# Performance work log

Hardware: AMD Instinct MI355X
Metric: run time of the kernel (lower is better)

## Reference

```python
import jax, jax.numpy as jnp
import numpy as np

D_MODEL = 1024
D_Q = 1024
D_K = 1024
D_V = 1024
B, S = 4, 2048


def setup_inputs() -> dict:
    key = jax.random.key(0)
    kx, kq, kk, kv = jax.random.split(key, 4)
    # torch Linear(in, out) weight is [out, in]; y = x @ W.T. Use kaiming-ish scale.
    sc = 1.0 / np.sqrt(D_MODEL)
    x = jax.random.normal(kx, (B, S, D_MODEL), dtype=jnp.float32)
    Wq = jax.random.normal(kq, (D_Q, D_MODEL), dtype=jnp.float32) * sc
    Wk = jax.random.normal(kk, (D_K, D_MODEL), dtype=jnp.float32) * sc
    Wv = jax.random.normal(kv, (D_V, D_MODEL), dtype=jnp.float32) * sc
    return {"x": x, "Wq": Wq, "Wk": Wk, "Wv": Wv}


def reference(x, Wq, Wk, Wv):
    d_k = Wk.shape[0]
    q = jnp.einsum('bsd,qd->bsq', x, Wq)  # [B,S,d_q]
    k = jnp.einsum('bsd,kd->bsk', x, Wk)  # [B,S,d_k]
    v = jnp.einsum('bsd,vd->bsv', x, Wv)  # [B,S,d_v]
    scores = jnp.einsum('bqd,bkd->bqk', q, k) / jnp.sqrt(jnp.float32(d_k))
    seq = scores.shape[-1]
    causal = jnp.tril(jnp.ones((seq, seq), dtype=bool))  # True = keep
    scores = jnp.where(causal[None, :, :], scores, -jnp.inf)
    probs = jax.nn.softmax(scores, axis=-1)
    return jnp.einsum('bqk,bkv->bqv', probs, v)
```

## Files before the change

kernel.cpp:

```cpp
#include <hip/hip_runtime.h>
#include <hip/hip_bf16.h>
#include <stdint.h>

typedef __attribute__((ext_vector_type(8))) short short8;
typedef __attribute__((ext_vector_type(4))) float floatx4;

typedef const __attribute__((address_space(1))) void* gvp;
typedef __attribute__((address_space(3))) void* lvp;

__device__ __forceinline__ unsigned short f2bf(float f) {
    unsigned u = __float_as_uint(f);
    u += 0x7fffu + ((u >> 16) & 1u);
    return (unsigned short)(u >> 16);
}

#define BAR()    do { asm volatile("" ::: "memory"); __builtin_amdgcn_s_barrier(); asm volatile("" ::: "memory"); } while (0)
#define WAITL()  do { asm volatile("s_waitcnt lgkmcnt(0)" ::: "memory"); __builtin_amdgcn_sched_barrier(0); } while (0)
#define WAITV4() asm volatile("s_waitcnt vmcnt(4)" ::: "memory")
#define WAITV0() asm volatile("s_waitcnt vmcnt(0)" ::: "memory")

__global__ __launch_bounds__(256)
void cvt_all(const float* __restrict__ x, const float* __restrict__ wq,
             const float* __restrict__ wk, const float* __restrict__ wv,
             unsigned short* __restrict__ Xb, unsigned short* __restrict__ WqT,
             unsigned short* __restrict__ WkT, unsigned short* __restrict__ Wvb) {
    const int b = blockIdx.x, t = threadIdx.x;
    if (b < 2304) {
        const float* in; unsigned short* out; long base;
        if (b < 2048) { in = x;  out = Xb;  base = (long)b * 1024; }
        else          { in = wv; out = Wvb; base = (long)(b - 2048) * 1024; }
        #pragma unroll
        for (int k = 0; k < 4; ++k) {
            long idx = base + k * 256 + t;
            float4 v = reinterpret_cast<const float4*>(in)[idx];
            uint2 o;
            o.x = (unsigned)f2bf(v.x) | ((unsigned)f2bf(v.y) << 16);
            o.y = (unsigned)f2bf(v.z) | ((unsigned)f2bf(v.w) << 16);
            reinterpret_cast<uint2*>(out)[idx] = o;
        }
    } else {
        const int bb = b - 2304;
        const float* in = (bb < 256) ? wq : wk;
        unsigned short* out = (bb < 256) ? WqT : WkT;
        const int tile = bb & 255;
        const int e0 = (tile >> 4) * 64, d0 = (tile & 15) * 64;
        __shared__ unsigned short ldsT[64][68];
        const int r = t >> 4, cq = t & 15;
        #pragma unroll
        for (int p = 0; p < 4; ++p) {
            const int e = p * 16 + r;
            float4 v = *reinterpret_cast<const float4*>(in + (long)(e0 + e) * 1024 + d0 + cq * 4);
            ldsT[cq*4+0][e] = f2bf(v.x);
            ldsT[cq*4+1][e] = f2bf(v.y);
            ldsT[cq*4+2][e] = f2bf(v.z);
            ldsT[cq*4+3][e] = f2bf(v.w);
        }
        __syncthreads();
        #pragma unroll
        for (int p = 0; p < 4; ++p) {
            const int d = p * 16 + r;
            ushort4 o = *reinterpret_cast<const ushort4*>(&ldsT[d][cq * 4]);
            *reinterpret_cast<ushort4*>(out + (long)(d0 + d) * 1024 + e0 + cq * 4) = o;
        }
    }
}

__device__ __forceinline__ void stage_tile(unsigned short* Abuf, unsigned short* Bbuf,
                                           const unsigned short* A, int lda,
                                           const unsigned short* B, int ldb, int k0,
                                           int wid, int srow, int piece) {
    #pragma unroll
    for (int i = 0; i < 4; ++i) {
        const int c = wid * 4 + i;
        const int row = c * 8 + srow;
        const int cs = (piece * 16) ^ ((row & 7) << 4);
        __builtin_amdgcn_global_load_lds(
            (gvp)(reinterpret_cast<const char*>(A + (long)row * lda + k0) + cs),
            (lvp)(reinterpret_cast<char*>(Abuf) + c * 1024), 16, 0, 0);
        __builtin_amdgcn_global_load_lds(
            (gvp)(reinterpret_cast<const char*>(B + (long)row * ldb + k0) + cs),
            (lvp)(reinterpret_cast<char*>(Bbuf) + c * 1024), 16, 0, 0);
    }
}

__device__ __forceinline__ void compute_tile(floatx4 acc[4][4], const unsigned short* As,
                                             const unsigned short* Bs, int wm, int wn,
                                             int frow, int lane) {
    #pragma unroll
    for (int ks = 0; ks < 2; ++ks) {
        short8 af[4], bf[4];
        const int colb = ks * 64 + (lane >> 4) * 16;
        #pragma unroll
        for (int i = 0; i < 4; ++i) {
            const int ar = wm + i * 16 + frow;
            af[i] = *reinterpret_cast<const short8*>(
                reinterpret_cast<const char*>(As) + ar * 128 + (colb ^ ((ar & 7) << 4)));
            const int br = wn + i * 16 + frow;
            bf[i] = *reinterpret_cast<const short8*>(
                reinterpret_cast<const char*>(Bs) + br * 128 + (colb ^ ((br & 7) << 4)));
        }
        #pragma unroll
        for (int i = 0; i < 4; ++i)
            #pragma unroll
            for (int j = 0; j < 4; ++j)
                acc[i][j] = __builtin_amdgcn_mfma_f32_16x16x32_bf16(af[i], bf[j], acc[i][j], 0, 0, 0);
    }
}

__global__ __launch_bounds__(256, 2)
void g_chunk(const unsigned short* __restrict__ WkT, const unsigned short* __restrict__ WqT,
             float* __restrict__ Gw) {
    const int bx = blockIdx.x, by = blockIdx.y, bz = blockIdx.z;
    const unsigned short* A = WkT + (long)by * 128 * 1024;
    const unsigned short* B = WqT + (long)bx * 128 * 1024;

    __shared__ unsigned short As[2][128 * 64];
    __shared__ unsigned short Bs[2][128 * 64];

    const int tid = threadIdx.x, lane = tid & 63, wid = tid >> 6;
    const int srow = lane >> 3, piece = lane & 7;
    const int wm = (wid >> 1) * 64, wn = (wid & 1) * 64, frow = lane & 15;

    floatx4 acc[4][4] = {};
    const int kbase = bz * 256;

    stage_tile(As[0], Bs[0], A, 1024, B, 1024, kbase, wid, srow, piece);
    WAITV0(); BAR();
    int cur = 0;
    #pragma unroll 1
    for (int t = 0; t < 4; ++t) {
        if (t < 3)
            stage_tile(As[cur ^ 1], Bs[cur ^ 1], A, 1024, B, 1024, kbase + (t + 1) * 64,
                       wid, srow, piece);
        compute_tile(acc, As[cur], Bs[cur], wm, wn, frow, lane);
        WAITV0(); BAR();
        cur ^= 1;
    }

    float* Cb = Gw + (long)bz * (1 << 20) + (long)(by * 128) * 1024 + bx * 128;
    const int cr0 = wm + (lane >> 4) * 4;
    const int cc0 = wn + (lane & 15);
    #pragma unroll
    for (int i = 0; i < 4; ++i)
        #pragma unroll
        for (int j = 0; j < 4; ++j)
            #pragma unroll
            for (int r = 0; r < 4; ++r)
                Cb[(long)(cr0 + i * 16 + r) * 1024 + cc0 + j * 16] = acc[i][j][r];
}

__global__ __launch_bounds__(256)
void reduce_g(const float* __restrict__ Gw, unsigned short* __restrict__ Gp) {
    const long i4 = (long)blockIdx.x * 256 + threadIdx.x;
    const long M4 = (1l << 20) / 4;
    float4 a = reinterpret_cast<const float4*>(Gw)[i4];
    float4 b = reinterpret_cast<const float4*>(Gw)[i4 + M4];
    float4 c = reinterpret_cast<const float4*>(Gw)[i4 + 2 * M4];
    float4 d = reinterpret_cast<const float4*>(Gw)[i4 + 3 * M4];
    float sx = (a.x + b.x + c.x + d.x) * 0.03125f;
    float sy = (a.y + b.y + c.y + d.y) * 0.03125f;
    float sz = (a.z + b.z + c.z + d.z) * 0.03125f;
    float sw = (a.w + b.w + c.w + d.w) * 0.03125f;
    uint2 o;
    o.x = (unsigned)f2bf(sx) | ((unsigned)f2bf(sy) << 16);
    o.y = (unsigned)f2bf(sz) | ((unsigned)f2bf(sw) << 16);
    reinterpret_cast<uint2*>(Gp)[i4] = o;
}

__global__ __launch_bounds__(256, 2)
void pv_sched(const unsigned short* __restrict__ P, const unsigned short* __restrict__ Vt,
              float* __restrict__ out) {
    const int flat = (blockIdx.z * 8 + blockIdx.y) * 8 + blockIdx.x;
    const int xcd = flat & 7, lid = flat >> 3;
    const int bz = xcd >> 1, parity = xcd & 1;
    const int bx = lid & 7;
    const int g  = lid >> 3;
    const int gi = (g < 4) ? g : (11 - g);
    const int by = parity + 2 * gi;

    const unsigned short* Pb = P + (long)bz * 2048 * 4096;
    const unsigned short* Bv = Vt + (long)bz * 1024 * 2048 + (long)(bx * 128) * 2048;
    const unsigned short* A = Pb + (long)by * 128 * 4096;
    float* Cb = out + (long)bz * 2048 * 1024;
    const int nt = (by + 1) * 2;

    __shared__ unsigned short As[2][128 * 64];
    __shared__ unsigned short Bs[2][128 * 64];

    const int tid = threadIdx.x, lane = tid & 63, wid = tid >> 6;
    const int srow = lane >> 3, piece = lane & 7;
    const int wm = (wid >> 1) * 64, wn = (wid & 1) * 64, frow = lane & 15;

    floatx4 acc[4][4] = {};
    stage_tile(As[0], Bs[0], A, 4096, Bv, 2048, 0, wid, srow, piece);
    WAITV0(); BAR();
    int cur = 0;
    #pragma unroll 1
    for (int t = 0; t < nt; ++t) {
        if (t + 1 < nt)
            stage_tile(As[cur ^ 1], Bs[cur ^ 1], A, 4096, Bv, 2048, (t + 1) * 64,
                       wid, srow, piece);
        compute_tile(acc, As[cur], Bs[cur], wm, wn, frow, lane);
        WAITV0(); BAR();
        cur ^= 1;
    }

    float* Cj = Cb + (long)(by * 128) * 1024 + bx * 128;
    const int cr0 = wm + (lane >> 4) * 4;
    const int cc0 = wn + (lane & 15);
    #pragma unroll
    for (int i = 0; i < 4; ++i)
        #pragma unroll
        for (int jj = 0; jj < 4; ++jj)
            #pragma unroll
            for (int r = 0; r < 4; ++r)
                Cj[(long)(cr0 + i * 16 + r) * 1024 + cc0 + jj * 16] = acc[i][jj][r];
}

__device__ __forceinline__ void stage_half(char* slot, const unsigned short* src,
                                           int ld, int k0, int tid) {
    #pragma unroll
    for (int r = 0; r < 2; ++r) {
        const int c = r * 512 + tid;
        const int row = c >> 3;
        const int cs = ((c & 7) * 16) ^ ((row & 7) << 4);
        const char* g = reinterpret_cast<const char*>(src + (long)row * ld + k0) + cs;
        __builtin_amdgcn_global_load_lds((gvp)g,
            (lvp)(slot + r * 8192 + (tid >> 6) * 1024), 16, 0, 0);
    }
}

__device__ __forceinline__ void load_a4(short8 a_[4][2], const char* slot, int mh,
                                        int fr, int csw0, int csw1) {
    #pragma unroll
    for (int i = 0; i < 4; ++i) {
        const int rb = (mh * 64 + i * 16 + fr) * 128;
        a_[i][0] = *reinterpret_cast<const short8*>(slot + rb + csw0);
        a_[i][1] = *reinterpret_cast<const short8*>(slot + rb + csw1);
    }
}

__device__ __forceinline__ void load_b2(short8 b_[2][2], const char* slot, int rbase,
                                        int nh, int fr, int csw0, int csw1) {
    #pragma unroll
    for (int j = 0; j < 2; ++j) {
        const int rb = (rbase + nh * 32 + j * 16 + fr) * 128;
        b_[j][0] = *reinterpret_cast<const short8*>(slot + rb + csw0);
        b_[j][1] = *reinterpret_cast<const short8*>(slot + rb + csw1);
    }
}

__device__ __forceinline__ void mfma16(floatx4 acc[8][4], short8 a_[4][2],
                                       short8 b_[2][2], int mh, int nh) {
    __builtin_amdgcn_s_setprio(1);
    #pragma unroll
    for (int i = 0; i < 4; ++i)
        #pragma unroll
        for (int j = 0; j < 2; ++j) {
            acc[mh*4+i][nh*2+j] = __builtin_amdgcn_mfma_f32_16x16x32_bf16(
                a_[i][0], b_[j][0], acc[mh*4+i][nh*2+j], 0, 0, 0);
            acc[mh*4+i][nh*2+j] = __builtin_amdgcn_mfma_f32_16x16x32_bf16(
                a_[i][1], b_[j][1], acc[mh*4+i][nh*2+j], 0, 0, 0);
        }
    __builtin_amdgcn_s_setprio(0);
}

template<typename CT, int MODE>
__global__ __launch_bounds__(512, 2)
void gemm8p(const unsigned short* __restrict__ A, const unsigned short* B,
            const unsigned short* B1, CT* __restrict__ C, unsigned short* __restrict__ Vt,
            int K, int lda, int ldb, int ldc,
            long sA, long sB, long sC, int nwg)
{
    const int gx = gridDim.x, gy = gridDim.y;
    int flat = (blockIdx.z * gy + blockIdx.y) * gx + blockIdx.x;
    int bx, by, bz = 0;
    bool isV = false;
    if (MODE == 1) {
        int xcd = flat & 7, lid = flat >> 3;
        int q = nwg >> 3, r = nwg & 7;
        flat = (xcd < r ? xcd * (q + 1) : r * (q + 1) + (xcd - r) * q) + lid;
        bx = flat % gx;
        int t2 = flat / gx;
        by = t2 % gy;
        bz = t2 / gy;
        if (bx > by) return;
    } else {
        const int xcd = flat & 7, lid = flat >> 3;
        by = xcd + ((lid >> 3) << 3);
        const int sub = lid & 7;
        isV = (sub >> 2) != 0;
        bx = sub & 3;
        if (isV) B = B1;
    }

    A += (long)bz * sA + (long)by * 256 * lda;
    B += (long)bz * sB + (long)bx * 256 * ldb;
    C += (long)bz * sC;

    __shared__ __align__(16) char lds[8 * 16384];
    #define SLOT(db, op, half) (lds + ((((db) << 1 | (op)) << 1 | (half)) * 16384))

    const int tid  = threadIdx.x;
    const int lane = tid & 63;
    const int wid  = tid >> 6;
    const int wm = wid >> 2;
    const int wn = wid & 3;
    const int bh = wn >> 1;
    const int brbase = (wn & 1) * 64;
    const int fr = lane & 15;
    const int csw0 = ((lane >> 4) * 16) ^ ((fr & 7) << 4);
    const int csw1 = (64 + (lane >> 4) * 16) ^ ((fr & 7) << 4);

    const unsigned short* Ah[2] = { A, A + 128ll * lda };
    const unsigned short* Bh[2] = { B, B + 128ll * ldb };

    const int NT = K >> 6;
    const int NI = NT >> 1;

    floatx4 acc[8][4] = {};
    short8 a_[4][2];
    short8 b_[2][2][2];

    stage_half(SLOT(0,1,0), Bh[0], ldb, 0, tid);
    stage_half(SLOT(0,1,1), Bh[1], ldb, 0, tid);
    stage_half(SLOT(0,0,0), Ah[0], lda, 0, tid);
    stage_half(SLOT(0,0,1), Ah[1], lda, 0, tid);
    stage_half(SLOT(1,1,0), Bh[0], ldb, 64, tid);
    stage_half(SLOT(1,1,1), Bh[1], ldb, 64, tid);
    WAITV4();
    BAR();

    for (int I = 0; I < NI; ++I) {
        const int kA1 = min(2*I + 1, NT - 1) * 64;
        const int kT2 = min(2*I + 2, NT - 1) * 64;
        const int kB3 = min(2*I + 3, NT - 1) * 64;

        load_a4(a_, SLOT(0,0,wm), 0, fr, csw0, csw1);
        load_b2(b_[0], SLOT(0,1,bh), brbase, 0, fr, csw0, csw1);
        stage_half(SLOT(1,0,0), Ah[0], lda, kA1, tid);
        BAR(); WAITL();
        mfma16(acc, a_, b_[0], 0, 0);
        BAR();

        load_b2(b_[1], SLOT(0,1,bh), brbase, 1, fr, csw0, csw1);
        stage_half(SLOT(1,0,1), Ah[1], lda, kA1, tid);
        BAR(); WAITL();
        mfma16(acc, a_, b_[1], 0, 1);
        BAR();

        load_a4(a_, SLOT(0,0,wm), 1, fr, csw0, csw1);
        stage_half(SLOT(0,1,0), Bh[0], ldb, kT2, tid);
        BAR(); WAITL();
        mfma16(acc, a_, b_[1], 1, 1);
        BAR();

        stage_half(SLOT(0,1,1), Bh[1], ldb, kT2, tid);
        BAR(); WAITL();
        mfma16(acc, a_, b_[0], 1, 0);
        WAITV4();
        BAR();

        load_a4(a_, SLOT(1,0,wm), 0, fr, csw0, csw1);
        load_b2(b_[0], SLOT(1,1,bh), brbase, 0, fr, csw0, csw1);
        stage_half(SLOT(0,0,0), Ah[0], lda, kT2, tid);
        BAR(); WAITL();
        mfma16(acc, a_, b_[0], 0, 0);
        BAR();

        load_b2(b_[1], SLOT(1,1,bh), brbase, 1, fr, csw0, csw1);
        stage_half(SLOT(0,0,1), Ah[1], lda, kT2, tid);
        BAR(); WAITL();
        mfma16(acc, a_, b_[1], 0, 1);
        BAR();

        load_a4(a_, SLOT(1,0,wm), 1, fr, csw0, csw1);
        stage_half(SLOT(1,1,0), Bh[0], ldb, kB3, tid);
        BAR(); WAITL();
        mfma16(acc, a_, b_[1], 1, 1);
        BAR();

        stage_half(SLOT(1,1,1), Bh[1], ldb, kB3, tid);
        BAR(); WAITL();
        mfma16(acc, a_, b_[0], 1, 0);
        WAITV4();
        BAR();
    }

    if (MODE == 3 && isV) {
        WAITV0();
        BAR();
        char* T = lds;
        #pragma unroll
        for (int i = 0; i < 8; ++i)
            #pragma unroll
            for (int j = 0; j < 4; ++j) {
                const int n = wn * 64 + j * 16 + fr;
                const int m = wm * 128 + ((lane >> 4) << 2) + i * 16;
                uint2 pk;
                pk.x = (unsigned)f2bf(acc[i][j][0]) | ((unsigned)f2bf(acc[i][j][1]) << 16);
                pk.y = (unsigned)f2bf(acc[i][j][2]) | ((unsigned)f2bf(acc[i][j][3]) << 16);
                *reinterpret_cast<uint2*>(T + n * 512 + ((m * 2) ^ ((n & 7) << 4))) = pk;
            }
        __syncthreads();
        const int b  = by >> 3;
        const int s0 = (by & 7) * 256;
        #pragma unroll
        for (int c = 0; c < 16; ++c) {
            const int idx = c * 512 + tid;
            const int n = idx >> 5, k = idx & 31;
            uint4 v = *reinterpret_cast<const uint4*>(T + n * 512 + ((k * 16) ^ ((n & 7) << 4)));
            *reinterpret_cast<uint4*>(Vt + (long)b * (1024 * 2048)
                + (long)(bx * 256 + n) * 2048 + s0 + k * 8) = v;
        }
        return;
    }

    const int cr0 = by * 256 + wm * 128 + (lane >> 4) * 4;
    const int cc0 = bx * 256 + wn * 64 + (lane & 15);
    #pragma unroll
    for (int i = 0; i < 8; ++i)
        #pragma unroll
        for (int j = 0; j < 4; ++j)
            #pragma unroll
            for (int r = 0; r < 4; ++r) {
                long idx = (long)(cr0 + i * 16 + r) * ldc + (cc0 + j * 16);
                float v = acc[i][j][r];
                if constexpr (sizeof(CT) == 4) C[idx] = v;
                else                           C[idx] = (CT)f2bf(v);
            }
    #undef SLOT
}

__global__ __launch_bounds__(256)
void softmax_causal(float* __restrict__ Sc) {
    const int b = blockIdx.y;
    const int t = threadIdx.x;
    const int lane = t & 63, wid = t >> 6;
    __shared__ float rmax[2][4], rsum[2][4];

    #pragma unroll 1
    for (int h = 0; h < 2; ++h) {
        const int q = h ? 2047 - blockIdx.x : blockIdx.x;
        float* row = Sc + ((long)b * 2048 + q) * 2048;
        const int kend = (q | 127) + 1;

        float vals[8];
        float mx = -INFINITY;
        #pragma unroll
        for (int i = 0; i < 2; ++i) {
            const int c0 = i * 1024 + t * 4;
            if (c0 <= q) {
                float4 v = *reinterpret_cast<const float4*>(row + c0);
                float tmp[4] = {v.x, v.y, v.z, v.w};
                #pragma unroll
                for (int j = 0; j < 4; ++j) {
                    float val = (c0 + j <= q) ? tmp[j] : -INFINITY;
                    vals[i * 4 + j] = val;
                    mx = fmaxf(mx, val);
                }
            } else {
                vals[i*4+0] = vals[i*4+1] = vals[i*4+2] = vals[i*4+3] = -INFINITY;
            }
        }
        #pragma unroll
        for (int o = 32; o > 0; o >>= 1) mx = fmaxf(mx, __shfl_xor(mx, o));
        if (lane == 0) rmax[h][wid] = mx;
        __syncthreads();
        mx = fmaxf(fmaxf(rmax[h][0], rmax[h][1]), fmaxf(rmax[h][2], rmax[h][3]));

        float s = 0.f;
        #pragma unroll
        for (int k = 0; k < 8; ++k) {
            float e = __expf(vals[k] - mx);
            vals[k] = e;
            s += e;
        }
        #pragma unroll
        for (int o = 32; o > 0; o >>= 1) s += __shfl_xor(s, o);
        if (lane == 0) rsum[h][wid] = s;
        __syncthreads();
        s = rsum[h][0] + rsum[h][1] + rsum[h][2] + rsum[h][3];
        const float inv = 1.f / s;

        unsigned short* orow = reinterpret_cast<unsigned short*>(row);
        #pragma unroll
        for (int i = 0; i < 2; ++i) {
            const int c0 = i * 1024 + t * 4;
            if (c0 < kend) {
                uint2 o;
                o.x = (unsigned)f2bf(vals[i*4+0] * inv) | ((unsigned)f2bf(vals[i*4+1] * inv) << 16);
                o.y = (unsigned)f2bf(vals[i*4+2] * inv) | ((unsigned)f2bf(vals[i*4+3] * inv) << 16);
                *reinterpret_cast<uint2*>(orow + c0) = o;
            }
        }
    }
}

extern "C" void kernel_launch(void* const* d_in, const int* in_sizes, int n_in,
                              void* d_out, int out_size, void* d_ws, size_t ws_size,
                              hipStream_t stream) {
    const float* x  = (const float*)d_in[0];
    const float* Wq = (const float*)d_in[1];
    const float* Wk = (const float*)d_in[2];
    const float* Wv = (const float*)d_in[3];
    float* out = (float*)d_out;

    char* w = (char*)d_ws;
    unsigned short* Xb  = (unsigned short*)(w);
    unsigned short* WqT = (unsigned short*)(w + (16ll << 20));
    unsigned short* WkT = (unsigned short*)(w + (18ll << 20));
    unsigned short* Wvb = (unsigned short*)(w + (20ll << 20));
    unsigned short* Yb  = (unsigned short*)(w + (22ll << 20));
    unsigned short* Gp  = (unsigned short*)(w + (38ll << 20));
    float*          Gw  = (float*)(w + (40ll << 20));
    unsigned short* Vt  = (unsigned short*)(w + (70ll << 20));
    float* Sc = (float*)(w + (86ll << 20));

    dim3 blk(256);
    cvt_all<<<2816, blk, 0, stream>>>(x, Wq, Wk, Wv, Xb, WqT, WkT, Wvb);

    g_chunk<<<dim3(8, 8, 4), blk, 0, stream>>>(WkT, WqT, Gw);
    reduce_g<<<1024, blk, 0, stream>>>(Gw, Gp);

    gemm8p<unsigned short, 3><<<dim3(256, 1, 1), dim3(512), 0, stream>>>(
        Xb, Gp, Wvb, Yb, Vt, 1024, 1024, 1024, 1024,
        0, 0, 0, 256);

    gemm8p<float, 1><<<dim3(8, 8, 4), dim3(512), 0, stream>>>(
        Yb, Xb, nullptr, Sc, nullptr, 1024, 1024, 1024, 2048,
        2048ll * 1024, 2048ll * 1024, 2048ll * 2048, 256);

    softmax_causal<<<dim3(1024, 4), blk, 0, stream>>>(Sc);

    pv_sched<<<dim3(8, 8, 8), blk, 0, stream>>>((const unsigned short*)Sc, Vt, out);
}
```

Baseline: 140.7 us.

## Compute Wk^T·Wq in one scaled GEMM launch and remap PV block order

Drops the split-K g_chunk kernel and its fp32 reduce pass. The Gram matrix is now computed directly by the existing 256x256-tile gemm8p in a new MODE 0, with the 1/sqrt(d) scale folded into its epilogue. This removes one launch and a 16 MB fp32 partial-sum round trip, but only 16 workgroups cover the 1024x1024x1024 product, leaving most CUs idle. The PV kernel gets a new block-index mapping that pairs rows from the two ends of the causal triangle. The vmcnt wait macros lose their memory clobbers, which lets the compiler reorder memory operations across the waits.

```diff
diff --git a/kernel.cpp b/kernel.cpp
--- a/kernel.cpp
+++ b/kernel.cpp
@@ -16,8 +16,8 @@
 
 #define BAR()    do { asm volatile("" ::: "memory"); __builtin_amdgcn_s_barrier(); asm volatile("" ::: "memory"); } while (0)
 #define WAITL()  do { asm volatile("s_waitcnt lgkmcnt(0)" ::: "memory"); __builtin_amdgcn_sched_barrier(0); } while (0)
-#define WAITV4() asm volatile("s_waitcnt vmcnt(4)" ::: "memory")
-#define WAITV0() asm volatile("s_waitcnt vmcnt(0)" ::: "memory")
+#define WAITV4() asm volatile("s_waitcnt vmcnt(4)")
+#define WAITV0() asm volatile("s_waitcnt vmcnt(0)")
 
 __global__ __launch_bounds__(256)
 void cvt_all(const float* __restrict__ x, const float* __restrict__ wq,
@@ -108,75 +108,15 @@
 }
 
 __global__ __launch_bounds__(256, 2)
-void g_chunk(const unsigned short* __restrict__ WkT, const unsigned short* __restrict__ WqT,
-             float* __restrict__ Gw) {
-    const int bx = blockIdx.x, by = blockIdx.y, bz = blockIdx.z;
-    const unsigned short* A = WkT + (long)by * 128 * 1024;
-    const unsigned short* B = WqT + (long)bx * 128 * 1024;
-
-    __shared__ unsigned short As[2][128 * 64];
-    __shared__ unsigned short Bs[2][128 * 64];
-
-    const int tid = threadIdx.x, lane = tid & 63, wid = tid >> 6;
-    const int srow = lane >> 3, piece = lane & 7;
-    const int wm = (wid >> 1) * 64, wn = (wid & 1) * 64, frow = lane & 15;
-
-    floatx4 acc[4][4] = {};
-    const int kbase = bz * 256;
-
-    stage_tile(As[0], Bs[0], A, 1024, B, 1024, kbase, wid, srow, piece);
-    WAITV0(); BAR();
-    int cur = 0;
-    #pragma unroll 1
-    for (int t = 0; t < 4; ++t) {
-        if (t < 3)
-            stage_tile(As[cur ^ 1], Bs[cur ^ 1], A, 1024, B, 1024, kbase + (t + 1) * 64,
-                       wid, srow, piece);
-        compute_tile(acc, As[cur], Bs[cur], wm, wn, frow, lane);
-        WAITV0(); BAR();
-        cur ^= 1;
-    }
-
-    float* Cb = Gw + (long)bz * (1 << 20) + (long)(by * 128) * 1024 + bx * 128;
-    const int cr0 = wm + (lane >> 4) * 4;
-    const int cc0 = wn + (lane & 15);
-    #pragma unroll
-    for (int i = 0; i < 4; ++i)
-        #pragma unroll
-        for (int j = 0; j < 4; ++j)
-            #pragma unroll
-            for (int r = 0; r < 4; ++r)
-                Cb[(long)(cr0 + i * 16 + r) * 1024 + cc0 + j * 16] = acc[i][j][r];
-}
-
-__global__ __launch_bounds__(256)
-void reduce_g(const float* __restrict__ Gw, unsigned short* __restrict__ Gp) {
-    const long i4 = (long)blockIdx.x * 256 + threadIdx.x;
-    const long M4 = (1l << 20) / 4;
-    float4 a = reinterpret_cast<const float4*>(Gw)[i4];
-    float4 b = reinterpret_cast<const float4*>(Gw)[i4 + M4];
-    float4 c = reinterpret_cast<const float4*>(Gw)[i4 + 2 * M4];
-    float4 d = reinterpret_cast<const float4*>(Gw)[i4 + 3 * M4];
-    float sx = (a.x + b.x + c.x + d.x) * 0.03125f;
-    float sy = (a.y + b.y + c.y + d.y) * 0.03125f;
-    float sz = (a.z + b.z + c.z + d.z) * 0.03125f;
-    float sw = (a.w + b.w + c.w + d.w) * 0.03125f;
-    uint2 o;
-    o.x = (unsigned)f2bf(sx) | ((unsigned)f2bf(sy) << 16);
-    o.y = (unsigned)f2bf(sz) | ((unsigned)f2bf(sw) << 16);
-    reinterpret_cast<uint2*>(Gp)[i4] = o;
-}
-
-__global__ __launch_bounds__(256, 2)
-void pv_sched(const unsigned short* __restrict__ P, const unsigned short* __restrict__ Vt,
-              float* __restrict__ out) {
+void pv_db(const unsigned short* __restrict__ P, const unsigned short* __restrict__ Vt,
+           float* __restrict__ out) {
     const int flat = (blockIdx.z * 8 + blockIdx.y) * 8 + blockIdx.x;
-    const int xcd = flat & 7, lid = flat >> 3;
-    const int bz = xcd >> 1, parity = xcd & 1;
-    const int bx = lid & 7;
-    const int g  = lid >> 3;
-    const int gi = (g < 4) ? g : (11 - g);
-    const int by = parity + 2 * gi;
+    const int half = flat >> 8;
+    const int r5   = flat & 255;
+    const int bx = r5 & 7;
+    const int pj = (r5 >> 3) & 7;
+    const int bz = r5 >> 6;
+    const int by = half ? 15 - pj : pj;
 
     const unsigned short* Pb = P + (long)bz * 2048 * 4096;
     const unsigned short* Bv = Vt + (long)bz * 1024 * 2048 + (long)(bx * 128) * 2048;
@@ -270,7 +210,7 @@
 void gemm8p(const unsigned short* __restrict__ A, const unsigned short* B,
             const unsigned short* B1, CT* __restrict__ C, unsigned short* __restrict__ Vt,
             int K, int lda, int ldb, int ldc,
-            long sA, long sB, long sC, int nwg)
+            long sA, long sB, long sC, int nwg, float csc)
 {
     const int gx = gridDim.x, gy = gridDim.y;
     int flat = (blockIdx.z * gy + blockIdx.y) * gx + blockIdx.x;
@@ -285,6 +225,9 @@
         by = t2 % gy;
         bz = t2 / gy;
         if (bx > by) return;
+    } else if (MODE == 0) {
+        bx = flat % gx;
+        by = flat / gx;
     } else {
         const int xcd = flat & 7, lid = flat >> 3;
         by = xcd + ((lid >> 3) << 3);
@@ -425,7 +368,7 @@
             #pragma unroll
             for (int r = 0; r < 4; ++r) {
                 long idx = (long)(cr0 + i * 16 + r) * ldc + (cc0 + j * 16);
-                float v = acc[i][j][r];
+                float v = acc[i][j][r] * csc;
                 if constexpr (sizeof(CT) == 4) C[idx] = v;
                 else                           C[idx] = (CT)f2bf(v);
             }
@@ -513,25 +456,25 @@
     unsigned short* Wvb = (unsigned short*)(w + (20ll << 20));
     unsigned short* Yb  = (unsigned short*)(w + (22ll << 20));
     unsigned short* Gp  = (unsigned short*)(w + (38ll << 20));
-    float*          Gw  = (float*)(w + (40ll << 20));
     unsigned short* Vt  = (unsigned short*)(w + (70ll << 20));
     float* Sc = (float*)(w + (86ll << 20));
 
     dim3 blk(256);
     cvt_all<<<2816, blk, 0, stream>>>(x, Wq, Wk, Wv, Xb, WqT, WkT, Wvb);
 
-    g_chunk<<<dim3(8, 8, 4), blk, 0, stream>>>(WkT, WqT, Gw);
-    reduce_g<<<1024, blk, 0, stream>>>(Gw, Gp);
+    gemm8p<unsigned short, 0><<<dim3(4, 4, 1), dim3(512), 0, stream>>>(
+        WkT, WqT, nullptr, Gp, nullptr, 1024, 1024, 1024, 1024,
+        0, 0, 0, 16, 0.03125f);
 
     gemm8p<unsigned short, 3><<<dim3(256, 1, 1), dim3(512), 0, stream>>>(
         Xb, Gp, Wvb, Yb, Vt, 1024, 1024, 1024, 1024,
-        0, 0, 0, 256);
+        0, 0, 0, 256, 1.0f);
 
     gemm8p<float, 1><<<dim3(8, 8, 4), dim3(512), 0, stream>>>(
         Yb, Xb, nullptr, Sc, nullptr, 1024, 1024, 1024, 2048,
-        2048ll * 1024, 2048ll * 1024, 2048ll * 2048, 256);
+        2048ll * 1024, 2048ll * 1024, 2048ll * 2048, 256, 1.0f);
 
     softmax_causal<<<dim3(1024, 4), blk, 0, stream>>>(Sc);
 
-    pv_sched<<<dim3(8, 8, 8), blk, 0, stream>>>((const unsigned short*)Sc, Vt, out);
-}
+    pv_db<<<dim3(8, 8, 8), blk, 0, stream>>>((const unsigned short*)Sc, Vt, out);
+}
```

Result: slower. 156.4 us (+11.2%).

## Widen PV kernel to 128x256 tiles with 512 threads and XCD remap

Applied to the files above, without the earlier changes.

Replaces the 128x128-tile, 256-thread PV GEMM with a 512-thread kernel computing 128x256 output tiles, inlining staging and MFMA compute with swizzled LDS and setprio around the MFMA block. Blocks are remapped so each XCD gets a contiguous group of tiles. The goal is more reuse of each P tile and fewer P reads from memory. In exchange there are fewer blocks (256), no explicit causal load balancing across rows, and the waitcnt macros lose their memory clobbers.

```diff
diff --git a/kernel.cpp b/kernel.cpp
--- a/kernel.cpp
+++ b/kernel.cpp
@@ -16,8 +16,8 @@
 
 #define BAR()    do { asm volatile("" ::: "memory"); __builtin_amdgcn_s_barrier(); asm volatile("" ::: "memory"); } while (0)
 #define WAITL()  do { asm volatile("s_waitcnt lgkmcnt(0)" ::: "memory"); __builtin_amdgcn_sched_barrier(0); } while (0)
-#define WAITV4() asm volatile("s_waitcnt vmcnt(4)" ::: "memory")
-#define WAITV0() asm volatile("s_waitcnt vmcnt(0)" ::: "memory")
+#define WAITV4() asm volatile("s_waitcnt vmcnt(4)")
+#define WAITV0() asm volatile("s_waitcnt vmcnt(0)")
 
 __global__ __launch_bounds__(256)
 void cvt_all(const float* __restrict__ x, const float* __restrict__ wq,
@@ -167,45 +167,86 @@
     reinterpret_cast<uint2*>(Gp)[i4] = o;
 }
 
-__global__ __launch_bounds__(256, 2)
-void pv_sched(const unsigned short* __restrict__ P, const unsigned short* __restrict__ Vt,
-              float* __restrict__ out) {
-    const int flat = (blockIdx.z * 8 + blockIdx.y) * 8 + blockIdx.x;
-    const int xcd = flat & 7, lid = flat >> 3;
-    const int bz = xcd >> 1, parity = xcd & 1;
-    const int bx = lid & 7;
-    const int g  = lid >> 3;
-    const int gi = (g < 4) ? g : (11 - g);
-    const int by = parity + 2 * gi;
-
-    const unsigned short* Pb = P + (long)bz * 2048 * 4096;
-    const unsigned short* Bv = Vt + (long)bz * 1024 * 2048 + (long)(bx * 128) * 2048;
-    const unsigned short* A = Pb + (long)by * 128 * 4096;
+__global__ __launch_bounds__(512, 1)
+void pv_wide(const unsigned short* __restrict__ P, const unsigned short* __restrict__ Vt,
+             float* __restrict__ out) {
+    int flat = (blockIdx.z * 16 + blockIdx.y) * 4 + blockIdx.x;
+    { int xcd = flat & 7, lid = flat >> 3; flat = xcd * 32 + lid; }
+    const int bx = flat & 3;
+    const int by = (flat >> 2) & 15;
+    const int bz = flat >> 6;
+
+    const unsigned short* A  = P  + (long)bz * 2048 * 4096 + (long)by * 128 * 4096;
+    const unsigned short* Bv = Vt + (long)bz * 1024 * 2048 + (long)(bx * 256) * 2048;
     float* Cb = out + (long)bz * 2048 * 1024;
     const int nt = (by + 1) * 2;
 
-    __shared__ unsigned short As[2][128 * 64];
-    __shared__ unsigned short Bs[2][128 * 64];
+    __shared__ __align__(16) unsigned short As[2][128 * 64];
+    __shared__ __align__(16) unsigned short Bs[2][256 * 64];
 
     const int tid = threadIdx.x, lane = tid & 63, wid = tid >> 6;
-    const int srow = lane >> 3, piece = lane & 7;
-    const int wm = (wid >> 1) * 64, wn = (wid & 1) * 64, frow = lane & 15;
+    const int wm = (wid >> 2) * 64;
+    const int wn = (wid & 3) * 64;
+    const int frow = lane & 15;
 
     floatx4 acc[4][4] = {};
-    stage_tile(As[0], Bs[0], A, 4096, Bv, 2048, 0, wid, srow, piece);
+
+    #define STAGE_WIDE(Ab, Bb, k0)                                                      \
+        do {                                                                            \
+            _Pragma("unroll")                                                           \
+            for (int r = 0; r < 2; ++r) {                                               \
+                const int c = r * 512 + tid;                                            \
+                const int row = c >> 3;                                                 \
+                const int cs = ((c & 7) * 16) ^ ((row & 7) << 4);                       \
+                __builtin_amdgcn_global_load_lds(                                       \
+                    (gvp)(reinterpret_cast<const char*>(A + (long)row * 4096 + (k0)) + cs), \
+                    (lvp)(reinterpret_cast<char*>(Ab) + r * 8192 + wid * 1024), 16, 0, 0); \
+            }                                                                           \
+            _Pragma("unroll")                                                           \
+            for (int r = 0; r < 4; ++r) {                                               \
+                const int c = r * 512 + tid;                                            \
+                const int row = c >> 3;                                                 \
+                const int cs = ((c & 7) * 16) ^ ((row & 7) << 4);                       \
+                __builtin_amdgcn_global_load_lds(                                       \
+                    (gvp)(reinterpret_cast<const char*>(Bv + (long)row * 2048 + (k0)) + cs), \
+                    (lvp)(reinterpret_cast<char*>(Bb) + r * 8192 + wid * 1024), 16, 0, 0); \
+            }                                                                           \
+        } while (0)
+
+    STAGE_WIDE(As[0], Bs[0], 0);
     WAITV0(); BAR();
     int cur = 0;
     #pragma unroll 1
     for (int t = 0; t < nt; ++t) {
         if (t + 1 < nt)
-            stage_tile(As[cur ^ 1], Bs[cur ^ 1], A, 4096, Bv, 2048, (t + 1) * 64,
-                       wid, srow, piece);
-        compute_tile(acc, As[cur], Bs[cur], wm, wn, frow, lane);
+            STAGE_WIDE(As[cur ^ 1], Bs[cur ^ 1], (t + 1) * 64);
+        #pragma unroll
+        for (int ks = 0; ks < 2; ++ks) {
+            short8 af[4], bf[4];
+            const int colb = ks * 64 + (lane >> 4) * 16;
+            #pragma unroll
+            for (int i = 0; i < 4; ++i) {
+                const int ar = wm + i * 16 + frow;
+                af[i] = *reinterpret_cast<const short8*>(
+                    reinterpret_cast<const char*>(As[cur]) + ar * 128 + (colb ^ ((ar & 7) << 4)));
+                const int br = wn + i * 16 + frow;
+                bf[i] = *reinterpret_cast<const short8*>(
+                    reinterpret_cast<const char*>(Bs[cur]) + br * 128 + (colb ^ ((br & 7) << 4)));
+            }
+            __builtin_amdgcn_s_setprio(1);
+            #pragma unroll
+            for (int i = 0; i < 4; ++i)
+                #pragma unroll
+                for (int j = 0; j < 4; ++j)
+                    acc[i][j] = __builtin_amdgcn_mfma_f32_16x16x32_bf16(af[i], bf[j], acc[i][j], 0, 0, 0);
+            __builtin_amdgcn_s_setprio(0);
+        }
         WAITV0(); BAR();
         cur ^= 1;
     }
-
-    float* Cj = Cb + (long)(by * 128) * 1024 + bx * 128;
+    #undef STAGE_WIDE
+
+    float* Cj = Cb + (long)(by * 128) * 1024 + bx * 256;
     const int cr0 = wm + (lane >> 4) * 4;
     const int cc0 = wn + (lane & 15);
     #pragma unroll
@@ -533,5 +574,5 @@
 
     softmax_causal<<<dim3(1024, 4), blk, 0, stream>>>(Sc);
 
-    pv_sched<<<dim3(8, 8, 8), blk, 0, stream>>>((const unsigned short*)Sc, Vt, out);
-}
+    pv_wide<<<dim3(4, 16, 4), dim3(512), 0, stream>>>((const unsigned short*)Sc, Vt, out);
+}
```

Result: slower. 148.4 us (+5.5%).
